# Kernel tuning notes

Hardware: AMD Instinct MI355X
Metric: run time of the kernel (lower is better)

Reference implementation:

```python
import jax, jax.numpy as jnp
import numpy as np

CLIP = 7.0          # cfg.swiglu_clip
AUX_COEF = 0.02     # cfg.router_aux_loss_coef
TOP_K = 4           # cfg.experts_per_token


def setup_inputs() -> dict:
    key = jax.random.key(0)
    ks = jax.random.split(key, 4)
    H, E, FF = 1024, 16, 1024
    B, T = 2, 1024
    std = 0.02
    return {
        "x": jax.random.normal(ks[0], (B, T, H), jnp.float32),
        "W_in": jax.random.normal(ks[1], (E, H, 2 * FF), jnp.float32) * std,
        "b_in": jnp.zeros((E, 2 * FF), jnp.float32),
        "W_out": jax.random.normal(ks[2], (E, FF, H), jnp.float32) * std,
        "b_out": jnp.zeros((E, H), jnp.float32),
        "router_w": jax.random.normal(ks[3], (E, H), jnp.float32) * std,
        "router_b": jnp.zeros((E,), jnp.float32),
    }


def reference(x, W_in, b_in, W_out, b_out, router_w, router_b):
    B, T, H = x.shape
    E = W_in.shape[0]
    S = B * T
    x_flat = x.reshape(S, H)

    # --- router + top-k gating ---
    logits = x_flat @ router_w.T + router_b                         # [S, E]
    topk_w, topk_i = jax.lax.top_k(logits, TOP_K)                   # [S, K]
    topk_w = jax.nn.softmax(topk_w.astype(jnp.float32), axis=-1).astype(x.dtype)

    # --- aux load-balance loss (faithful to source, incl. argmax-over-indices) ---
    probs = jax.nn.softmax(logits.astype(jnp.float32), axis=-1)     # [S, E]
    importance = probs.mean(axis=0)                                 # [E]
    load = jax.nn.one_hot(jnp.argmax(topk_i, axis=-1), E, dtype=jnp.float32).mean(axis=0)
    aux_loss = AUX_COEF * E * jnp.sum(importance * load)

    # scatter top-k weights to dense [S, E] combine weights
    final_w = jnp.zeros((S, E), x.dtype).at[jnp.arange(S)[:, None], topk_i].add(topk_w)

    # --- dense per-expert SwiGLU FFN (every expert for every token) ---
    h = jnp.einsum('sh,ehd->sed', x_flat, W_in) + b_in              # [S, E, 2*FF]
    up, gate = jnp.split(h, 2, axis=-1)                             # chunk(2, -1)
    up = jnp.clip(up, -CLIP, CLIP)
    gate = jnp.clip(gate, -CLIP, CLIP)
    act = jax.nn.silu(gate) * up                                    # [S, E, FF]
    eo = jnp.einsum('sef,efh->seh', act, W_out) + b_out             # [S, E, H]

    out = jnp.einsum('seh,se->sh', eo, final_w).reshape(B, T, H)
    return out, aux_loss
```

## Files before the change

### kernel.cpp

```cpp
#include <hip/hip_runtime.h>
#include <math.h>

#define S_TOK 2048
#define H_DIM 1024
#define E_NUM 16
#define FF_DIM 1024
#define TOPK 4
#define CLIPV 7.0f
#define AUXC 0.02f
#define BK 32
#define NT (H_DIM / BK)

typedef short bf16x8 __attribute__((ext_vector_type(8)));
typedef float f32x4 __attribute__((ext_vector_type(4)));

__device__ __forceinline__ unsigned short f2bf(float f) {
  unsigned int u = __float_as_uint(f);
  u += 0x7fffu + ((u >> 16) & 1u);
  return (unsigned short)(u >> 16);
}

__device__ __forceinline__ void gload16(const void* g, void* l) {
  __builtin_amdgcn_global_load_lds((const __attribute__((address_space(1))) void*)g,
                                   (__attribute__((address_space(3))) void*)l, 16, 0, 0);
}

__device__ __forceinline__ int imin(int a, int b) { return a < b ? a : b; }

__global__ void logits_kernel(const float* __restrict__ x, const float* __restrict__ rw,
                              const float* __restrict__ rb, float* __restrict__ logits,
                              unsigned short* __restrict__ xb) {
  int tok = blockIdx.x * 4 + (threadIdx.x >> 6);
  int lane = threadIdx.x & 63;
  const float4* xr = (const float4*)(x + (size_t)tok * H_DIM);
  ushort4* xbw = (ushort4*)(xb + (size_t)tok * H_DIM);
  float p[E_NUM];
#pragma unroll
  for (int e = 0; e < E_NUM; ++e) p[e] = 0.f;
#pragma unroll
  for (int it = 0; it < 4; ++it) {
    float4 xv = xr[it * 64 + lane];
    ushort4 o;
    o.x = f2bf(xv.x); o.y = f2bf(xv.y); o.z = f2bf(xv.z); o.w = f2bf(xv.w);
    xbw[it * 64 + lane] = o;
#pragma unroll
    for (int e = 0; e < E_NUM; ++e) {
      float4 wv = ((const float4*)(rw + (size_t)e * H_DIM))[it * 64 + lane];
      p[e] += xv.x * wv.x + xv.y * wv.y + xv.z * wv.z + xv.w * wv.w;
    }
  }
#pragma unroll
  for (int e = 0; e < E_NUM; ++e) {
#pragma unroll
    for (int off = 32; off > 0; off >>= 1) p[e] += __shfl_xor(p[e], off);
  }
  if (lane == 0) {
    float4* lp = (float4*)&logits[tok * E_NUM];
#pragma unroll
    for (int q = 0; q < 4; ++q)
      lp[q] = make_float4(p[q * 4 + 0] + rb[q * 4 + 0], p[q * 4 + 1] + rb[q * 4 + 1],
                          p[q * 4 + 2] + rb[q * 4 + 2], p[q * 4 + 3] + rb[q * 4 + 3]);
  }
}

__global__ __launch_bounds__(256) void topk_kernel(const float* __restrict__ logits,
                                                   int* __restrict__ topk_i, float* __restrict__ topk_w,
                                                   int* __restrict__ counts, float* __restrict__ imp,
                                                   int* __restrict__ pos_cnt) {
  __shared__ float s_imp[E_NUM];
  __shared__ int s_cnt[E_NUM];
  __shared__ int s_pos[TOPK];
  int tid = threadIdx.x;
  if (tid < E_NUM) { s_imp[tid] = 0.f; s_cnt[tid] = 0; }
  if (tid < TOPK) s_pos[tid] = 0;
  __syncthreads();

  int t = blockIdx.x * 256 + tid;
  float lg[E_NUM];
  {
    const float4* lp = (const float4*)&logits[t * E_NUM];
#pragma unroll
    for (int q = 0; q < 4; ++q) {
      float4 v = lp[q];
      lg[q * 4 + 0] = v.x; lg[q * 4 + 1] = v.y; lg[q * 4 + 2] = v.z; lg[q * 4 + 3] = v.w;
    }
  }
  int idx[TOPK]; float val[TOPK];
  float tmp[E_NUM];
#pragma unroll
  for (int e = 0; e < E_NUM; ++e) tmp[e] = lg[e];
#pragma unroll
  for (int k = 0; k < TOPK; ++k) {
    float best = -INFINITY; int bi = 0;
#pragma unroll
    for (int e = 0; e < E_NUM; ++e) if (tmp[e] > best) { best = tmp[e]; bi = e; }
    val[k] = best; idx[k] = bi; tmp[bi] = -INFINITY;
  }
  float ssum = 0.f, wv[TOPK];
#pragma unroll
  for (int k = 0; k < TOPK; ++k) { wv[k] = expf(val[k] - val[0]); ssum += wv[k]; }
#pragma unroll
  for (int k = 0; k < TOPK; ++k) wv[k] /= ssum;
#pragma unroll
  for (int k = 0; k < TOPK; ++k) {
    topk_i[t * TOPK + k] = idx[k];
    topk_w[t * TOPK + k] = wv[k];
  }
  float se = 0.f, pr[E_NUM];
#pragma unroll
  for (int e = 0; e < E_NUM; ++e) { pr[e] = expf(lg[e] - val[0]); se += pr[e]; }
  float inv = 1.f / se;
  int mi = idx[0], pos = 0;
#pragma unroll
  for (int k = 1; k < TOPK; ++k) if (idx[k] > mi) { mi = idx[k]; pos = k; }

  int lane = tid & 63;
#pragma unroll
  for (int e = 0; e < E_NUM; ++e) {
    float v = pr[e] * inv;
    int c = (idx[0] == e) + (idx[1] == e) + (idx[2] == e) + (idx[3] == e);
#pragma unroll
    for (int off = 32; off > 0; off >>= 1) {
      v += __shfl_xor(v, off);
      c += __shfl_xor(c, off);
    }
    if (lane == 0) {
      atomicAdd(&s_imp[e], v);
      atomicAdd(&s_cnt[e], c);
    }
  }
#pragma unroll
  for (int k = 0; k < TOPK; ++k) {
    int pc = (pos == k) ? 1 : 0;
#pragma unroll
    for (int off = 32; off > 0; off >>= 1) pc += __shfl_xor(pc, off);
    if (lane == 0) atomicAdd(&s_pos[k], pc);
  }
  __syncthreads();
  if (tid < E_NUM) {
    atomicAdd(&imp[tid], s_imp[tid]);
    atomicAdd(&counts[tid], s_cnt[tid]);
  }
  if (tid < TOPK) atomicAdd(&pos_cnt[tid], s_pos[tid]);
}

__global__ void scan_kernel(const int* __restrict__ counts, int* __restrict__ offsets) {
  if (threadIdx.x == 0) {
    int off = 0;
    for (int e = 0; e < E_NUM; ++e) { offsets[e] = off; off += counts[e]; }
    offsets[E_NUM] = off;
  }
}

__global__ __launch_bounds__(256) void assign_kernel(
    const int* __restrict__ topk_i, const int* __restrict__ offsets, int* __restrict__ cursor,
    int* __restrict__ tok_list, int* __restrict__ slot_of) {
  __shared__ int s_cnt[E_NUM];
  __shared__ int s_base[E_NUM];
  int tid = threadIdx.x;
  if (tid < E_NUM) s_cnt[tid] = 0;
  __syncthreads();
  int t = blockIdx.x * 256 + tid;
  int e[TOPK], lslot[TOPK];
#pragma unroll
  for (int k = 0; k < TOPK; ++k) {
    e[k] = topk_i[t * TOPK + k];
    lslot[k] = atomicAdd(&s_cnt[e[k]], 1);
  }
  __syncthreads();
  if (tid < E_NUM) s_base[tid] = atomicAdd(&cursor[tid], s_cnt[tid]);
  __syncthreads();
#pragma unroll
  for (int k = 0; k < TOPK; ++k) {
    int slot = offsets[e[k]] + s_base[e[k]] + lslot[k];
    tok_list[slot] = t;
    slot_of[t * TOPK + k] = slot;
  }
}

__global__ void transpose_kernel(const float* __restrict__ in, unsigned short* __restrict__ out,
                                 int R, int C) {
  __shared__ float tile[64][65];
  int e = blockIdx.z;
  in  += (size_t)e * R * C;
  out += (size_t)e * R * C;
  int r0 = blockIdx.y * 64, c0 = blockIdx.x * 64;
  int tx = threadIdx.x & 15, ty = threadIdx.x >> 4;
#pragma unroll
  for (int j = 0; j < 4; ++j) {
    int r = ty + j * 16;
    float4 v = *(const float4*)&in[(size_t)(r0 + r) * C + c0 + tx * 4];
    tile[r][tx * 4 + 0] = v.x; tile[r][tx * 4 + 1] = v.y;
    tile[r][tx * 4 + 2] = v.z; tile[r][tx * 4 + 3] = v.w;
  }
  __syncthreads();
#pragma unroll
  for (int j = 0; j < 4; ++j) {
    int c = ty + j * 16;
    ushort4 o;
    o.x = f2bf(tile[tx * 4 + 0][c]);
    o.y = f2bf(tile[tx * 4 + 1][c]);
    o.z = f2bf(tile[tx * 4 + 2][c]);
    o.w = f2bf(tile[tx * 4 + 3][c]);
    *(ushort4*)&out[(size_t)(c0 + c) * R + r0 + tx * 4] = o;
  }
}

__global__ __launch_bounds__(256, 6) void gemm1_kernel(
    const unsigned short* __restrict__ xb, const unsigned short* __restrict__ winT,
    const float* __restrict__ b_in, const int* __restrict__ offsets,
    const int* __restrict__ tok_list, unsigned short* __restrict__ act) {
  __shared__ unsigned short ldsA[2][128 * BK];
  __shared__ unsigned short ldsB[2][64 * BK];
  const int lin = blockIdx.x;
  const int nid = (lin & 7) * 1024 + (lin >> 3);
  const int e  = nid >> 9;
  const int nt = (nid >> 4) & 31;
  const int mt = nid & 15;
  const int base = offsets[e];
  const int cnt = offsets[e + 1] - base;
  if (mt * 128 >= cnt) return;
  const int n0f = nt * 32;
  const int tid = threadIdx.x, w = tid >> 6, lane = tid & 63;

  const int arow = w * 16 + (lane >> 2);
  const int t0 = tok_list[base + imin(mt * 128 + arow, cnt - 1)];
  const int t1 = tok_list[base + imin(mt * 128 + arow + 64, cnt - 1)];
  const unsigned short* gA0 = xb + (size_t)t0 * H_DIM + (lane & 3) * 8;
  const unsigned short* gA1 = xb + (size_t)t1 * H_DIM + (lane & 3) * 8;
  const int rB = arow;
  const int fB = n0f + ((rB >> 5) << 4) + (rB & 15);
  const int wrow = ((rB >> 4) & 1) ? (FF_DIM + fB) : fB;
  const unsigned short* we = winT + (size_t)e * 2 * FF_DIM * H_DIM;
  const unsigned short* gB0 = we + (size_t)wrow * H_DIM + (lane & 3) * 8;

  f32x4 acc[4][2];
#pragma unroll
  for (int m = 0; m < 4; ++m)
#pragma unroll
    for (int n = 0; n < 2; ++n) acc[m][n] = (f32x4){0.f, 0.f, 0.f, 0.f};

#define STAGE1(buf, k0)                                        \
  do {                                                         \
    gload16(gA0 + (k0), &ldsA[buf][(w * 16) * BK]);            \
    gload16(gA1 + (k0), &ldsA[buf][(w * 16 + 64) * BK]);       \
    gload16(gB0 + (k0), &ldsB[buf][(w * 16) * BK]);            \
  } while (0)

  STAGE1(0, 0);
  __syncthreads();
  int buf = 0;
  const int ko = (lane >> 4) * 8;
  const int wm = (w >> 1) * 64, wn = (w & 1) * 32;
  for (int kt = 0; kt < NT; ++kt) {
    if (kt + 1 < NT) STAGE1(buf ^ 1, (kt + 1) * BK);
    bf16x8 a[4], b[2];
#pragma unroll
    for (int mf = 0; mf < 4; ++mf)
      a[mf] = *(const bf16x8*)&ldsA[buf][(wm + mf * 16 + (lane & 15)) * BK + ko];
#pragma unroll
    for (int nf = 0; nf < 2; ++nf)
      b[nf] = *(const bf16x8*)&ldsB[buf][(wn + nf * 16 + (lane & 15)) * BK + ko];
#pragma unroll
    for (int mf = 0; mf < 4; ++mf)
#pragma unroll
      for (int nf = 0; nf < 2; ++nf)
        acc[mf][nf] = __builtin_amdgcn_mfma_f32_16x16x32_bf16(a[mf], b[nf], acc[mf][nf], 0, 0, 0);
    __syncthreads();
    buf ^= 1;
  }

  const float* bin = b_in + (size_t)e * 2 * FF_DIM;
  const int f = n0f + (w & 1) * 16 + (lane & 15);
  const float bu = bin[f], bg = bin[FF_DIM + f];
#pragma unroll
  for (int mf = 0; mf < 4; ++mf) {
    int rbase = wm + mf * 16 + (lane >> 4) * 4;
#pragma unroll
    for (int i = 0; i < 4; ++i) {
      int mrow = mt * 128 + rbase + i;
      if (mrow < cnt) {
        float up = acc[mf][0][i] + bu;
        float gt = acc[mf][1][i] + bg;
        up = fminf(fmaxf(up, -CLIPV), CLIPV);
        gt = fminf(fmaxf(gt, -CLIPV), CLIPV);
        float av = (gt / (1.f + expf(-gt))) * up;
        act[(size_t)(base + mrow) * FF_DIM + f] = f2bf(av);
      }
    }
  }
}

__global__ __launch_bounds__(256, 6) void gemm2_kernel(
    const unsigned short* __restrict__ act, const unsigned short* __restrict__ woutT,
    const float* __restrict__ b_out, const int* __restrict__ offsets,
    float* __restrict__ eo) {
  __shared__ unsigned short ldsA[2][128 * BK];
  __shared__ unsigned short ldsB[2][64 * BK];
  const int lin = blockIdx.x;
  const int nid = (lin & 7) * 512 + (lin >> 3);
  const int e = nid >> 8;
  const int nt = (nid >> 4) & 15;
  const int mt = nid & 15;
  const int base = offsets[e];
  const int cnt = offsets[e + 1] - base;
  if (mt * 128 >= cnt) return;
  const int n0 = nt * 64;
  const int tid = threadIdx.x, w = tid >> 6, lane = tid & 63;

  const int arow = w * 16 + (lane >> 2);
  const int m0_ = imin(mt * 128 + arow, cnt - 1);
  const int m1_ = imin(mt * 128 + arow + 64, cnt - 1);
  const unsigned short* gA0 = act + (size_t)(base + m0_) * FF_DIM + (lane & 3) * 8;
  const unsigned short* gA1 = act + (size_t)(base + m1_) * FF_DIM + (lane & 3) * 8;
  const unsigned short* we = woutT + (size_t)e * H_DIM * FF_DIM;
  const unsigned short* gB0 = we + (size_t)(n0 + arow) * FF_DIM + (lane & 3) * 8;

  f32x4 acc[4][2];
#pragma unroll
  for (int m = 0; m < 4; ++m)
#pragma unroll
    for (int n = 0; n < 2; ++n) acc[m][n] = (f32x4){0.f, 0.f, 0.f, 0.f};

#define STAGE2(buf, k0)                                        \
  do {                                                         \
    gload16(gA0 + (k0), &ldsA[buf][(w * 16) * BK]);            \
    gload16(gA1 + (k0), &ldsA[buf][(w * 16 + 64) * BK]);       \
    gload16(gB0 + (k0), &ldsB[buf][(w * 16) * BK]);            \
  } while (0)

  STAGE2(0, 0);
  __syncthreads();
  int buf = 0;
  const int ko = (lane >> 4) * 8;
  const int wm = (w >> 1) * 64, wn = (w & 1) * 32;
  for (int kt = 0; kt < FF_DIM / BK; ++kt) {
    if (kt + 1 < FF_DIM / BK) STAGE2(buf ^ 1, (kt + 1) * BK);
    bf16x8 a[4], b[2];
#pragma unroll
    for (int mf = 0; mf < 4; ++mf)
      a[mf] = *(const bf16x8*)&ldsA[buf][(wm + mf * 16 + (lane & 15)) * BK + ko];
#pragma unroll
    for (int nf = 0; nf < 2; ++nf)
      b[nf] = *(const bf16x8*)&ldsB[buf][(wn + nf * 16 + (lane & 15)) * BK + ko];
#pragma unroll
    for (int mf = 0; mf < 4; ++mf)
#pragma unroll
      for (int nf = 0; nf < 2; ++nf)
        acc[mf][nf] = __builtin_amdgcn_mfma_f32_16x16x32_bf16(a[mf], b[nf], acc[mf][nf], 0, 0, 0);
    __syncthreads();
    buf ^= 1;
  }

  const float* bo = b_out + (size_t)e * H_DIM;
#pragma unroll
  for (int mf = 0; mf < 4; ++mf) {
#pragma unroll
    for (int i = 0; i < 4; ++i) {
      int mrow = mt * 128 + wm + mf * 16 + (lane >> 4) * 4 + i;
      if (mrow < cnt) {
        float* row = eo + (size_t)(base + mrow) * H_DIM;
#pragma unroll
        for (int nf = 0; nf < 2; ++nf) {
          int h = n0 + wn + nf * 16 + (lane & 15);
          row[h] = acc[mf][nf][i] + bo[h];
        }
      }
    }
  }
}

__global__ __launch_bounds__(256) void combine_kernel(
    const float* __restrict__ eo, const float* __restrict__ topk_w,
    const int* __restrict__ slot_of, float* __restrict__ out) {
  int t = blockIdx.x;
  int tid = threadIdx.x;
  float4 r = make_float4(0.f, 0.f, 0.f, 0.f);
#pragma unroll
  for (int k = 0; k < TOPK; ++k) {
    int s = slot_of[t * TOPK + k];
    float wv = topk_w[t * TOPK + k];
    float4 v = ((const float4*)(eo + (size_t)s * H_DIM))[tid];
    r.x = fmaf(wv, v.x, r.x);
    r.y = fmaf(wv, v.y, r.y);
    r.z = fmaf(wv, v.z, r.z);
    r.w = fmaf(wv, v.w, r.w);
  }
  ((float4*)(out + (size_t)t * H_DIM))[tid] = r;
}

__global__ void finalize_kernel(const float* __restrict__ imp, const int* __restrict__ pos_cnt,
                                float* __restrict__ out_aux) {
  if (threadIdx.x == 0) {
    float s = 0.f;
    for (int p = 0; p < TOPK; ++p)
      s += (imp[p] / (float)S_TOK) * ((float)pos_cnt[p] / (float)S_TOK);
    *out_aux = AUXC * (float)E_NUM * s;
  }
}

extern "C" void kernel_launch(void* const* d_in, const int* in_sizes, int n_in,
                              void* d_out, int out_size, void* d_ws, size_t ws_size,
                              hipStream_t stream) {
  const float* x     = (const float*)d_in[0];
  const float* W_in  = (const float*)d_in[1];
  const float* b_in  = (const float*)d_in[2];
  const float* W_out = (const float*)d_in[3];
  const float* b_out = (const float*)d_in[4];
  const float* rw    = (const float*)d_in[5];
  const float* rb    = (const float*)d_in[6];
  float* out = (float*)d_out;

  char* ws = (char*)d_ws;
  size_t off = 0;
  auto alloc = [&](size_t bytes) {
    void* p = ws + off;
    off = (off + bytes + 255) & ~(size_t)255;
    return p;
  };
  unsigned short* xb    = (unsigned short*)alloc((size_t)S_TOK * H_DIM * 2);
  unsigned short* winT  = (unsigned short*)alloc((size_t)E_NUM * 2 * FF_DIM * H_DIM * 2);
  unsigned short* woutT = (unsigned short*)alloc((size_t)E_NUM * H_DIM * FF_DIM * 2);
  unsigned short* act   = (unsigned short*)alloc((size_t)S_TOK * TOPK * FF_DIM * 2);
  float* eo      = (float*)alloc((size_t)S_TOK * TOPK * H_DIM * 4);
  float* logits  = (float*)alloc((size_t)S_TOK * E_NUM * 4);
  int*   topk_i  = (int*)alloc(S_TOK * TOPK * 4);
  float* topk_w  = (float*)alloc(S_TOK * TOPK * 4);
  int*   tok_list= (int*)alloc(S_TOK * TOPK * 4);
  int*   slot_of = (int*)alloc(S_TOK * TOPK * 4);
  int* ctrl = (int*)alloc(64 * 4);
  int* counts = ctrl;
  int* cursor = ctrl + 16;
  int* pos_cnt = ctrl + 32;
  float* imp = (float*)(ctrl + 48);
  int* offsets = (int*)alloc(32 * 4);

  hipMemsetAsync(ctrl, 0, 64 * 4, stream);

  logits_kernel<<<S_TOK / 4, 256, 0, stream>>>(x, rw, rb, logits, xb);
  transpose_kernel<<<dim3(2 * FF_DIM / 64, H_DIM / 64, E_NUM), 256, 0, stream>>>(W_in, winT, H_DIM, 2 * FF_DIM);
  transpose_kernel<<<dim3(H_DIM / 64, FF_DIM / 64, E_NUM), 256, 0, stream>>>(W_out, woutT, FF_DIM, H_DIM);
  topk_kernel<<<S_TOK / 256, 256, 0, stream>>>(logits, topk_i, topk_w, counts, imp, pos_cnt);
  scan_kernel<<<1, 64, 0, stream>>>(counts, offsets);
  assign_kernel<<<S_TOK / 256, 256, 0, stream>>>(topk_i, offsets, cursor, tok_list, slot_of);
  gemm1_kernel<<<8192, 256, 0, stream>>>(xb, winT, b_in, offsets, tok_list, act);
  gemm2_kernel<<<4096, 256, 0, stream>>>(act, woutT, b_out, offsets, eo);
  combine_kernel<<<S_TOK, 256, 0, stream>>>(eo, topk_w, slot_of, out);
  finalize_kernel<<<1, 64, 0, stream>>>(imp, pos_cnt, out + (size_t)S_TOK * H_DIM);
}
```

Baseline: 201.5 us.

## Fuse small kernels into neighbours and widen gemm2 tile to 128x128

Folds the expert-offset scan into assign_kernel, merges the two weight transposes into one launch, and moves the aux-loss finalize into combine_kernel, removing three kernel launches and the gaps between them. gemm2 now uses 128x128 output tiles (four B fragments per wave, launch bounds lowered to 4 blocks), which doubles reuse of each A tile from LDS. The cost is more registers and LDS per block, fewer blocks for skewed experts, and a redundant serial scan in every assign block.

```diff
diff --git a/kernel.cpp b/kernel.cpp
--- a/kernel.cpp
+++ b/kernel.cpp
@@ -144,20 +144,21 @@
   if (tid < TOPK) atomicAdd(&pos_cnt[tid], s_pos[tid]);
 }
 
-__global__ void scan_kernel(const int* __restrict__ counts, int* __restrict__ offsets) {
-  if (threadIdx.x == 0) {
-    int off = 0;
-    for (int e = 0; e < E_NUM; ++e) { offsets[e] = off; off += counts[e]; }
-    offsets[E_NUM] = off;
-  }
-}
-
 __global__ __launch_bounds__(256) void assign_kernel(
-    const int* __restrict__ topk_i, const int* __restrict__ offsets, int* __restrict__ cursor,
-    int* __restrict__ tok_list, int* __restrict__ slot_of) {
+    const int* __restrict__ topk_i, const int* __restrict__ counts, int* __restrict__ cursor,
+    int* __restrict__ tok_list, int* __restrict__ slot_of, int* __restrict__ offsets) {
   __shared__ int s_cnt[E_NUM];
   __shared__ int s_base[E_NUM];
+  __shared__ int s_off[E_NUM + 1];
   int tid = threadIdx.x;
+  if (tid == 0) {
+    int o = 0;
+    for (int e2 = 0; e2 < E_NUM; ++e2) { s_off[e2] = o; o += counts[e2]; }
+    s_off[E_NUM] = o;
+    if (blockIdx.x == 0) {
+      for (int e2 = 0; e2 <= E_NUM; ++e2) offsets[e2] = s_off[e2];
+    }
+  }
   if (tid < E_NUM) s_cnt[tid] = 0;
   __syncthreads();
   int t = blockIdx.x * 256 + tid;
@@ -172,19 +173,36 @@
   __syncthreads();
 #pragma unroll
   for (int k = 0; k < TOPK; ++k) {
-    int slot = offsets[e[k]] + s_base[e[k]] + lslot[k];
+    int slot = s_off[e[k]] + s_base[e[k]] + lslot[k];
     tok_list[slot] = t;
     slot_of[t * TOPK + k] = slot;
   }
 }
 
-__global__ void transpose_kernel(const float* __restrict__ in, unsigned short* __restrict__ out,
-                                 int R, int C) {
+__global__ void transpose_fused_kernel(const float* __restrict__ W_in, unsigned short* __restrict__ winT,
+                                       const float* __restrict__ W_out, unsigned short* __restrict__ woutT) {
   __shared__ float tile[64][65];
-  int e = blockIdx.z;
-  in  += (size_t)e * R * C;
-  out += (size_t)e * R * C;
-  int r0 = blockIdx.y * 64, c0 = blockIdx.x * 64;
+  const int bid = blockIdx.x;
+  const float* in;
+  unsigned short* out;
+  int C, r0, c0;
+  if (bid < 8192) {
+    int e = bid >> 9, rem = bid & 511;
+    in  = W_in  + (size_t)e * H_DIM * 2 * FF_DIM;
+    out = winT  + (size_t)e * H_DIM * 2 * FF_DIM;
+    C = 2 * FF_DIM;
+    c0 = (rem & 31) * 64;
+    r0 = (rem >> 5) * 64;
+  } else {
+    int b = bid - 8192;
+    int e = b >> 8, rem = b & 255;
+    in  = W_out + (size_t)e * FF_DIM * H_DIM;
+    out = woutT + (size_t)e * FF_DIM * H_DIM;
+    C = H_DIM;
+    c0 = (rem & 15) * 64;
+    r0 = (rem >> 4) * 64;
+  }
+  const int R_out = (bid < 8192) ? H_DIM : FF_DIM;
   int tx = threadIdx.x & 15, ty = threadIdx.x >> 4;
 #pragma unroll
   for (int j = 0; j < 4; ++j) {
@@ -202,7 +220,7 @@
     o.y = f2bf(tile[tx * 4 + 1][c]);
     o.z = f2bf(tile[tx * 4 + 2][c]);
     o.w = f2bf(tile[tx * 4 + 3][c]);
-    *(ushort4*)&out[(size_t)(c0 + c) * R + r0 + tx * 4] = o;
+    *(ushort4*)&out[(size_t)(c0 + c) * R_out + r0 + tx * 4] = o;
   }
 }
 
@@ -291,62 +309,65 @@
   }
 }
 
-__global__ __launch_bounds__(256, 6) void gemm2_kernel(
+__global__ __launch_bounds__(256, 4) void gemm2_kernel(
     const unsigned short* __restrict__ act, const unsigned short* __restrict__ woutT,
     const float* __restrict__ b_out, const int* __restrict__ offsets,
     float* __restrict__ eo) {
   __shared__ unsigned short ldsA[2][128 * BK];
-  __shared__ unsigned short ldsB[2][64 * BK];
+  __shared__ unsigned short ldsB[2][128 * BK];
   const int lin = blockIdx.x;
-  const int nid = (lin & 7) * 512 + (lin >> 3);
-  const int e = nid >> 8;
-  const int nt = (nid >> 4) & 15;
+  const int nid = (lin & 7) * 256 + (lin >> 3);
+  const int e = nid >> 7;
+  const int nt = (nid >> 4) & 7;
   const int mt = nid & 15;
   const int base = offsets[e];
   const int cnt = offsets[e + 1] - base;
   if (mt * 128 >= cnt) return;
-  const int n0 = nt * 64;
+  const int n0 = nt * 128;
   const int tid = threadIdx.x, w = tid >> 6, lane = tid & 63;
 
-  const int arow = w * 16 + (lane >> 2);
-  const int m0_ = imin(mt * 128 + arow, cnt - 1);
-  const int m1_ = imin(mt * 128 + arow + 64, cnt - 1);
+  const int srow0 = w * 32 + (lane >> 2);
+  const int srow1 = srow0 + 16;
+  const int m0_ = imin(mt * 128 + srow0, cnt - 1);
+  const int m1_ = imin(mt * 128 + srow1, cnt - 1);
   const unsigned short* gA0 = act + (size_t)(base + m0_) * FF_DIM + (lane & 3) * 8;
   const unsigned short* gA1 = act + (size_t)(base + m1_) * FF_DIM + (lane & 3) * 8;
   const unsigned short* we = woutT + (size_t)e * H_DIM * FF_DIM;
-  const unsigned short* gB0 = we + (size_t)(n0 + arow) * FF_DIM + (lane & 3) * 8;
-
-  f32x4 acc[4][2];
+  const unsigned short* gB0 = we + (size_t)(n0 + srow0) * FF_DIM + (lane & 3) * 8;
+  const unsigned short* gB1 = we + (size_t)(n0 + srow1) * FF_DIM + (lane & 3) * 8;
+
+  f32x4 acc[4][4];
 #pragma unroll
   for (int m = 0; m < 4; ++m)
 #pragma unroll
-    for (int n = 0; n < 2; ++n) acc[m][n] = (f32x4){0.f, 0.f, 0.f, 0.f};
+    for (int n = 0; n < 4; ++n) acc[m][n] = (f32x4){0.f, 0.f, 0.f, 0.f};
 
 #define STAGE2(buf, k0)                                        \
   do {                                                         \
-    gload16(gA0 + (k0), &ldsA[buf][(w * 16) * BK]);            \
-    gload16(gA1 + (k0), &ldsA[buf][(w * 16 + 64) * BK]);       \
-    gload16(gB0 + (k0), &ldsB[buf][(w * 16) * BK]);            \
+    gload16(gA0 + (k0), &ldsA[buf][(w * 32 + 0) * BK]);        \
+    gload16(gA1 + (k0), &ldsA[buf][(w * 32 + 16) * BK]);       \
+    gload16(gB0 + (k0), &ldsB[buf][(w * 32 + 0) * BK]);        \
+    gload16(gB1 + (k0), &ldsB[buf][(w * 32 + 16) * BK]);       \
   } while (0)
 
   STAGE2(0, 0);
   __syncthreads();
   int buf = 0;
   const int ko = (lane >> 4) * 8;
-  const int wm = (w >> 1) * 64, wn = (w & 1) * 32;
+  const int wm = (w >> 1) * 64, wn = (w & 1) * 64;
   for (int kt = 0; kt < FF_DIM / BK; ++kt) {
     if (kt + 1 < FF_DIM / BK) STAGE2(buf ^ 1, (kt + 1) * BK);
-    bf16x8 a[4], b[2];
+    bf16x8 a[4], b[4];
 #pragma unroll
     for (int mf = 0; mf < 4; ++mf)
       a[mf] = *(const bf16x8*)&ldsA[buf][(wm + mf * 16 + (lane & 15)) * BK + ko];
 #pragma unroll
-    for (int nf = 0; nf < 2; ++nf)
+    for (int nf = 0; nf < 4; ++nf)
       b[nf] = *(const bf16x8*)&ldsB[buf][(wn + nf * 16 + (lane & 15)) * BK + ko];
 #pragma unroll
     for (int mf = 0; mf < 4; ++mf)
 #pragma unroll
-      for (int nf = 0; nf < 2; ++nf)
+      for (int nf = 0; nf < 4; ++nf)
         acc[mf][nf] = __builtin_amdgcn_mfma_f32_16x16x32_bf16(a[mf], b[nf], acc[mf][nf], 0, 0, 0);
     __syncthreads();
     buf ^= 1;
@@ -361,7 +382,7 @@
       if (mrow < cnt) {
         float* row = eo + (size_t)(base + mrow) * H_DIM;
 #pragma unroll
-        for (int nf = 0; nf < 2; ++nf) {
+        for (int nf = 0; nf < 4; ++nf) {
           int h = n0 + wn + nf * 16 + (lane & 15);
           row[h] = acc[mf][nf][i] + bo[h];
         }
@@ -372,7 +393,8 @@
 
 __global__ __launch_bounds__(256) void combine_kernel(
     const float* __restrict__ eo, const float* __restrict__ topk_w,
-    const int* __restrict__ slot_of, float* __restrict__ out) {
+    const int* __restrict__ slot_of, float* __restrict__ out,
+    const float* __restrict__ imp, const int* __restrict__ pos_cnt) {
   int t = blockIdx.x;
   int tid = threadIdx.x;
   float4 r = make_float4(0.f, 0.f, 0.f, 0.f);
@@ -387,15 +409,11 @@
     r.w = fmaf(wv, v.w, r.w);
   }
   ((float4*)(out + (size_t)t * H_DIM))[tid] = r;
-}
-
-__global__ void finalize_kernel(const float* __restrict__ imp, const int* __restrict__ pos_cnt,
-                                float* __restrict__ out_aux) {
-  if (threadIdx.x == 0) {
+  if (t == 0 && tid == 0) {
     float s = 0.f;
     for (int p = 0; p < TOPK; ++p)
       s += (imp[p] / (float)S_TOK) * ((float)pos_cnt[p] / (float)S_TOK);
-    *out_aux = AUXC * (float)E_NUM * s;
+    out[(size_t)S_TOK * H_DIM] = AUXC * (float)E_NUM * s;
   }
 }
 
@@ -438,13 +456,10 @@
   hipMemsetAsync(ctrl, 0, 64 * 4, stream);
 
   logits_kernel<<<S_TOK / 4, 256, 0, stream>>>(x, rw, rb, logits, xb);
-  transpose_kernel<<<dim3(2 * FF_DIM / 64, H_DIM / 64, E_NUM), 256, 0, stream>>>(W_in, winT, H_DIM, 2 * FF_DIM);
-  transpose_kernel<<<dim3(H_DIM / 64, FF_DIM / 64, E_NUM), 256, 0, stream>>>(W_out, woutT, FF_DIM, H_DIM);
+  transpose_fused_kernel<<<12288, 256, 0, stream>>>(W_in, winT, W_out, woutT);
   topk_kernel<<<S_TOK / 256, 256, 0, stream>>>(logits, topk_i, topk_w, counts, imp, pos_cnt);
-  scan_kernel<<<1, 64, 0, stream>>>(counts, offsets);
-  assign_kernel<<<S_TOK / 256, 256, 0, stream>>>(topk_i, offsets, cursor, tok_list, slot_of);
+  assign_kernel<<<S_TOK / 256, 256, 0, stream>>>(topk_i, counts, cursor, tok_list, slot_of, offsets);
   gemm1_kernel<<<8192, 256, 0, stream>>>(xb, winT, b_in, offsets, tok_list, act);
-  gemm2_kernel<<<4096, 256, 0, stream>>>(act, woutT, b_out, offsets, eo);
-  combine_kernel<<<S_TOK, 256, 0, stream>>>(eo, topk_w, slot_of, out);
-  finalize_kernel<<<1, 64, 0, stream>>>(imp, pos_cnt, out + (size_t)S_TOK * H_DIM);
-}
+  gemm2_kernel<<<2048, 256, 0, stream>>>(act, woutT, b_out, offsets, eo);
+  combine_kernel<<<S_TOK, 256, 0, stream>>>(eo, topk_w, slot_of, out, imp, pos_cnt);
+}
```

After: 200.3 us. About the same (-0.6%).
